# Kernel tuning notes

Hardware: AMD Instinct MI355X
Metric: run time of the kernel (lower is better)

## Reference

```python
import jax, jax.numpy as jnp
import numpy as np

N = 50000       # nodes
E = 600000      # directed edges (before self loops)
IN_CH = 128
HID = 64
HEADS = 2
H2_CH = HID // HEADS  # 32
OUT_CH = 96
NEG_SLOPE = 0.2


def _w(key, shape):
    fan_in = shape[-1]
    return jax.random.normal(key, shape, dtype=jnp.float32) / np.sqrt(fan_in).astype(np.float32)


def setup_inputs() -> dict:
    key = jax.random.key(0)
    ks = jax.random.split(key, 20)
    x = jax.random.normal(ks[0], (N, IN_CH), dtype=jnp.float32)
    edge_index = jax.random.randint(ks[1], (2, E), 0, N, dtype=jnp.int32)
    batch = jnp.zeros((N,), dtype=jnp.int32)
    return {
        "x": x, "edge_index": edge_index, "batch": batch,
        # lin_in 128->128
        "Win": _w(ks[2], (IN_CH, IN_CH)), "b_in": jnp.zeros((IN_CH,), jnp.float32),
        # conv1: GATv2Conv(128 -> 64, heads=2, concat=True)
        "Wl1": _w(ks[3], (HEADS * HID, IN_CH)), "bl1": jnp.zeros((HEADS * HID,), jnp.float32),
        "Wr1": _w(ks[4], (HEADS * HID, IN_CH)), "br1": jnp.zeros((HEADS * HID,), jnp.float32),
        "att1": _w(ks[5], (HEADS, HID)), "bias1": jnp.zeros((HEADS * HID,), jnp.float32),
        # conv2: GATv2Conv(128 -> 32, heads=1, concat=True)
        "Wl2": _w(ks[6], (H2_CH, HEADS * HID)), "bl2": jnp.zeros((H2_CH,), jnp.float32),
        "Wr2": _w(ks[7], (H2_CH, HEADS * HID)), "br2": jnp.zeros((H2_CH,), jnp.float32),
        "att2": _w(ks[8], (1, H2_CH)), "bias2": jnp.zeros((H2_CH,), jnp.float32),
        # final linear 32 -> 96
        "Wout": _w(ks[9], (OUT_CH, H2_CH)), "b_out": jnp.zeros((OUT_CH,), jnp.float32),
    }


def _segment_softmax(logits, seg, num):
    # logits: [E, H] grouped by seg (destination node); every node has a self loop.
    m = jax.ops.segment_max(logits, seg, num_segments=num)
    ex = jnp.exp(logits - m[seg])
    s = jax.ops.segment_sum(ex, seg, num_segments=num)
    return ex / s[seg]


def _gatv2_conv(h, Wl, bl, Wr, br, att, bias, src, dst, heads, ch):
    n = h.shape[0]
    xl = (h @ Wl.T + bl).reshape(n, heads, ch)  # source-side (x_j)
    xr = (h @ Wr.T + br).reshape(n, heads, ch)  # target-side (x_i)
    e = jax.nn.leaky_relu(xl[src] + xr[dst], NEG_SLOPE)       # [E, H, C]
    logits = jnp.einsum('ehc,hc->eh', e, att)                  # [E, H]
    alpha = _segment_softmax(logits, dst, n)                   # softmax over in-edges per dst
    out = jax.ops.segment_sum(alpha[:, :, None] * xl[src], dst, num_segments=n)
    return out.reshape(n, heads * ch) + bias


def reference(x, edge_index, batch, Win, b_in, Wl1, bl1, Wr1, br1, att1, bias1,
              Wl2, bl2, Wr2, br2, att2, bias2, Wout, b_out):
    n = x.shape[0]
    loops = jnp.arange(n, dtype=edge_index.dtype)
    src = jnp.concatenate([edge_index[0], loops])  # add_self_loops=True (PyG default)
    dst = jnp.concatenate([edge_index[1], loops])
    h = x @ Win.T + b_in
    h = jax.nn.relu(_gatv2_conv(h, Wl1, bl1, Wr1, br1, att1, bias1, src, dst, HEADS, HID))
    h = jax.nn.relu(_gatv2_conv(h, Wl2, bl2, Wr2, br2, att2, bias2, src, dst, 1, H2_CH))
    num_graphs = 1
    sums = jax.ops.segment_sum(h, batch, num_segments=num_graphs)          # [G, 32]
    cnt = jax.ops.segment_sum(jnp.ones((n,), h.dtype), batch, num_segments=num_graphs)
    pooled = sums / cnt[:, None]
    return pooled @ Wout.T + b_out  # [G, 96]
```

## Files before the change

kernel.cpp:

```cpp
#include <hip/hip_runtime.h>
#include <hip/hip_bf16.h>
#include <math.h>


#define NEG_SLOPE 0.2f
#define LOG2E 1.4426950408889634f
#define NREP 16
#define ELLW 64
#define CH 2048
#define CAPB 8192

typedef __attribute__((ext_vector_type(8))) short bf16x8;
typedef __attribute__((ext_vector_type(4))) float f32x4;

__device__ __forceinline__ float leaky(float t) { return fmaxf(t, NEG_SLOPE * t); }
__device__ __forceinline__ float bf2f(unsigned short u) {
    return __uint_as_float((unsigned)u << 16);
}
__device__ __forceinline__ short f2bf(float f) {
    __hip_bfloat16 h = __float2bfloat16(f);
    return *reinterpret_cast<short*>(&h);
}
__device__ __forceinline__ short f2bf_fast(float f) {
    return (short)((__float_as_uint(f) + 0x8000u) >> 16);
}

template <int CTRL>
__device__ __forceinline__ float dppadd(float v) {
    int t = __builtin_amdgcn_update_dpp(0, __float_as_int(v), CTRL, 0xF, 0xF, true);
    return v + __int_as_float(t);
}

__global__ __launch_bounds__(256) void prep_kernel(const float* __restrict__ Win,
                                                   const float* __restrict__ b_in,
                                                   const float* __restrict__ Wl1,
                                                   const float* __restrict__ bl1,
                                                   const float* __restrict__ Wr1,
                                                   const float* __restrict__ br1,
                                                   const float* __restrict__ Wl2,
                                                   const float* __restrict__ bl2,
                                                   const float* __restrict__ Wr2,
                                                   const float* __restrict__ br2,
                                                   unsigned short* __restrict__ Wcat1,
                                                   float* __restrict__ bcat1,
                                                   unsigned short* __restrict__ Wcat2,
                                                   float* __restrict__ bcat2,
                                                   int* __restrict__ bucketCnt,
                                                   float* __restrict__ pooledR, int N) {
    int b = blockIdx.x, t = threadIdx.x;
    if (b < 128) {
        int half = t >> 7;
        int k = t & 127;
        int o = b * 2 + half;
        const float* Wx = (o < 128) ? Wl1 : Wr1;
        const float* bx = (o < 128) ? bl1 : br1;
        int oo = o & 127;
        float acc = 0.f;
#pragma unroll 16
        for (int j = 0; j < 128; ++j)
            acc = fmaf(Wx[oo * 128 + j], Win[j * 128 + k], acc);
        Wcat1[o * 128 + k] = (unsigned short)f2bf(acc);

        __shared__ float red[256];
        red[t] = Wx[oo * 128 + k] * b_in[k];
        __syncthreads();
        for (int off = 64; off > 0; off >>= 1) {
            if (k < off) red[t] += red[t + off];
            __syncthreads();
        }
        if (k == 0) bcat1[o] = red[half * 128] + bx[oo];
    } else if (b < 160) {
        int i = (b - 128) * 256 + t;
        int m = i >> 7, kk = i & 127;
        float v = (m < 32) ? Wl2[m * 128 + kk] : Wr2[(m - 32) * 128 + kk];
        Wcat2[i] = (unsigned short)f2bf(v);
        if (b == 128 && t < 64) bcat2[t] = (t < 32) ? bl2[t] : br2[t - 32];
    } else if (b == 160) {
        if (t < 256) bucketCnt[t] = 0;
    } else {
        int i = (b - 161) * 256 + t;
        if (i < NREP * 32) pooledR[i] = 0.f;
    }
}

__device__ __forceinline__ void gemm1_body(const float* __restrict__ x,
                                           const unsigned short* __restrict__ W,
                                           const float* __restrict__ bias,
                                           unsigned short* __restrict__ XL,
                                           unsigned short* __restrict__ XR,
                                           int N, int nb) {
    const int w = threadIdx.x >> 6;
    const int lane = threadIdx.x & 63;
    const int ln = lane & 15;
    const int quad = lane >> 4;
    const int c0 = w * 64;

    int rows[2];
#pragma unroll
    for (int rt = 0; rt < 2; ++rt) {
        int n = nb + rt * 16 + ln;
        rows[rt] = n < N ? n : N - 1;
    }

    float4 araw[2][4][2];
#pragma unroll
    for (int rt = 0; rt < 2; ++rt)
#pragma unroll
        for (int kc = 0; kc < 4; ++kc) {
            const float* p = x + (size_t)rows[rt] * 128 + kc * 32 + quad * 8;
            araw[rt][kc][0] = *(const float4*)p;
            araw[rt][kc][1] = *(const float4*)(p + 4);
        }
    bf16x8 a[2][4];
#pragma unroll
    for (int rt = 0; rt < 2; ++rt)
#pragma unroll
        for (int kc = 0; kc < 4; ++kc) {
            float4 u = araw[rt][kc][0], v = araw[rt][kc][1];
            a[rt][kc][0] = f2bf_fast(u.x); a[rt][kc][1] = f2bf_fast(u.y);
            a[rt][kc][2] = f2bf_fast(u.z); a[rt][kc][3] = f2bf_fast(u.w);
            a[rt][kc][4] = f2bf_fast(v.x); a[rt][kc][5] = f2bf_fast(v.y);
            a[rt][kc][6] = f2bf_fast(v.z); a[rt][kc][7] = f2bf_fast(v.w);
        }

    f32x4 acc[2][4];
#pragma unroll
    for (int rt = 0; rt < 2; ++rt)
#pragma unroll
        for (int ct = 0; ct < 4; ++ct) acc[rt][ct] = (f32x4){0.f, 0.f, 0.f, 0.f};

#pragma unroll
    for (int kc = 0; kc < 4; ++kc) {
        const int k0 = kc * 32 + quad * 8;
        bf16x8 wv[4];
#pragma unroll
        for (int ct = 0; ct < 4; ++ct)
            wv[ct] = *(const bf16x8*)(W + (size_t)(c0 + ct * 16 + ln) * 128 + k0);
#pragma unroll
        for (int rt = 0; rt < 2; ++rt)
#pragma unroll
            for (int ct = 0; ct < 4; ++ct)
                acc[rt][ct] = __builtin_amdgcn_mfma_f32_16x16x32_bf16(wv[ct], a[rt][kc], acc[rt][ct], 0, 0, 0);
    }

#pragma unroll
    for (int rt = 0; rt < 2; ++rt) {
        int n = nb + rt * 16 + ln;
        if (n >= N) continue;
#pragma unroll
        for (int ct = 0; ct < 4; ++ct) {
            int cb = c0 + ct * 16 + quad * 4;
            float4 bv = *(const float4*)&bias[cb];
            ushort4 o;
            o.x = (unsigned short)f2bf(acc[rt][ct][0] + bv.x);
            o.y = (unsigned short)f2bf(acc[rt][ct][1] + bv.y);
            o.z = (unsigned short)f2bf(acc[rt][ct][2] + bv.z);
            o.w = (unsigned short)f2bf(acc[rt][ct][3] + bv.w);
            if (cb < 128) *(ushort4*)&XL[(size_t)n * 128 + cb] = o;
            else          *(ushort4*)&XR[(size_t)n * 128 + cb - 128] = o;
        }
    }
}

__global__ __launch_bounds__(256) void fuse1_kernel(const int* __restrict__ ei,
                                                    int* __restrict__ bucketCnt,
                                                    unsigned int* __restrict__ region,
                                                    int E,
                                                    const float* __restrict__ x,
                                                    const unsigned short* __restrict__ W,
                                                    const float* __restrict__ bias,
                                                    unsigned short* __restrict__ XL,
                                                    unsigned short* __restrict__ XR,
                                                    int N, int PB) {
    __shared__ int hist[256];
    __shared__ int base[256];
    __shared__ int off[256];
    if (blockIdx.x >= PB) {
        gemm1_body(x, W, bias, XL, XR, N, (blockIdx.x - PB) * 32);
        return;
    }
    int b = blockIdx.x, t = threadIdx.x;
    int e0 = b * CH;
    int e1 = e0 + CH; if (e1 > E) e1 = E;

    hist[t] = 0;
    __syncthreads();
    for (int e = e0 + t; e < e1; e += 256) {
        int d = ei[E + e];
        atomicAdd(&hist[d >> 8], 1);
    }
    __syncthreads();
    int h = hist[t];
    base[t] = (h > 0) ? atomicAdd(&bucketCnt[t], h) : 0;
    off[t] = 0;
    __syncthreads();
    for (int e = e0 + t; e < e1; e += 256) {
        int s = ei[e];
        int d = ei[E + e];
        int bk = d >> 8;
        int p = base[bk] + atomicAdd(&off[bk], 1);
        if (p < CAPB)
            region[(size_t)bk * CAPB + p] = (unsigned)s | ((unsigned)(d & 255) << 16);
    }
}

__global__ __launch_bounds__(256) void fuse2_kernel(const unsigned int* __restrict__ region,
                                                    const int* __restrict__ bucketCnt,
                                                    unsigned short* __restrict__ ell,
                                                    int* __restrict__ deg,
                                                    const float* __restrict__ x,
                                                    const unsigned short* __restrict__ W,
                                                    const float* __restrict__ bias,
                                                    unsigned short* __restrict__ XL,
                                                    unsigned short* __restrict__ XR,
                                                    int N, int NB, int nodeOff) {
    __shared__ unsigned short tile[256 * ELLW];
    __shared__ int cur[256];
    if (blockIdx.x >= NB) {
        gemm1_body(x, W, bias, XL, XR, N, nodeOff + (blockIdx.x - NB) * 32);
        return;
    }
    int nb = blockIdx.x, t = threadIdx.x;
    cur[t] = 0;
    __syncthreads();
    int cnt = bucketCnt[nb];
    if (cnt > CAPB) cnt = CAPB;
    for (int i = t; i < cnt; i += 256) {
        unsigned p = region[(size_t)nb * CAPB + i];
        int doff = p >> 16;
        int s = p & 0xFFFF;
        int r = atomicAdd(&cur[doff], 1);
        if (r < ELLW) tile[doff * ELLW + r] = (unsigned short)s;
    }
    __syncthreads();
    int node = nb * 256 + t;
    int dgl = cur[t];
    if (dgl > ELLW) dgl = ELLW;
    if (node < N) {
        deg[node] = dgl;
        int pe = dgl + 8; if (pe > ELLW) pe = ELLW;
        for (int r = dgl; r < pe; ++r) tile[t * ELLW + r] = (unsigned short)node;
    }
    __syncthreads();
    const uint4* tl = (const uint4*)tile;
    uint4* gl = (uint4*)(ell + (size_t)nb * 256 * ELLW);
#pragma unroll
    for (int k = 0; k < 8; ++k) {
        int idx = t + k * 256;
        int row = idx >> 3;
        if (nb * 256 + row < N) gl[idx] = tl[idx];
    }
}

__global__ __launch_bounds__(256) void node_conv1(const unsigned short* __restrict__ XL,
                                                  const unsigned short* __restrict__ XR,
                                                  const int* __restrict__ deg,
                                                  const unsigned short* __restrict__ ell,
                                                  const float* __restrict__ att,
                                                  const float* __restrict__ bias,
                                                  const unsigned short* __restrict__ Wcat2,
                                                  const float* __restrict__ bcat2,
                                                  unsigned short* __restrict__ XL2,
                                                  unsigned short* __restrict__ XR2, int N) {
    __shared__ unsigned short hsh[8 * 128];
    int g = threadIdx.x >> 5;
    int d = blockIdx.x * 8 + g;
    int l = threadIdx.x & 31;
    int c0 = 4 * l;

    if (d < N) {
        const unsigned short* row = ell + (size_t)d * ELLW;
        int re = deg[d];

        float4 attv = *(const float4*)&att[c0];
        attv.x *= LOG2E; attv.y *= LOG2E; attv.z *= LOG2E; attv.w *= LOG2E;
        ushort4 xru = *(const ushort4*)&XR[(size_t)d * 128 + c0];
        float xr0 = bf2f(xru.x), xr1 = bf2f(xru.y), xr2 = bf2f(xru.z), xr3 = bf2f(xru.w);

        float ssum, a0, a1, a2, a3;
        float w_self, xs0, xs1, xs2, xs3;

#define LOADX1(s) (*(const ushort4*)&XL[(size_t)(s) * 128 + c0])
#define PROC1(xu)                                                          \
    {                                                                      \
        float x0 = bf2f(xu.x), x1 = bf2f(xu.y), x2 = bf2f(xu.z), x3 = bf2f(xu.w); \
        float p = leaky(x0 + xr0) * attv.x;                                \
        p = fmaf(leaky(x1 + xr1), attv.y, p);                              \
        p = fmaf(leaky(x2 + xr2), attv.z, p);                              \
        p = fmaf(leaky(x3 + xr3), attv.w, p);                              \
        p = dppadd<0xB1>(p);                                               \
        p = dppadd<0x4E>(p);                                               \
        p = dppadd<0x124>(p);                                              \
        p = dppadd<0x128>(p);                                              \
        float wgt = exp2f(p);                                              \
        ssum += wgt;                                                       \
        a0 = fmaf(wgt, x0, a0); a1 = fmaf(wgt, x1, a1);                    \
        a2 = fmaf(wgt, x2, a2); a3 = fmaf(wgt, x3, a3);                    \
    }

        {
            ushort4 xu = *(const ushort4*)&XL[(size_t)d * 128 + c0];
            xs0 = bf2f(xu.x); xs1 = bf2f(xu.y); xs2 = bf2f(xu.z); xs3 = bf2f(xu.w);
            float p = leaky(xs0 + xr0) * attv.x;
            p = fmaf(leaky(xs1 + xr1), attv.y, p);
            p = fmaf(leaky(xs2 + xr2), attv.z, p);
            p = fmaf(leaky(xs3 + xr3), attv.w, p);
            p = dppadd<0xB1>(p);
            p = dppadd<0x4E>(p);
            p = dppadd<0x124>(p);
            p = dppadd<0x128>(p);
            w_self = exp2f(p);
            ssum = w_self;
            a0 = w_self * xs0; a1 = w_self * xs1;
            a2 = w_self * xs2; a3 = w_self * xs3;
        }
        if (re > 0) {
            int rp = (re + 3) & ~3;
            ushort4 i0 = *(const ushort4*)&row[0];
            ushort4 b0 = LOADX1(i0.x), b1 = LOADX1(i0.y), b2 = LOADX1(i0.z), b3 = LOADX1(i0.w);
            for (int j = 0; j < rp; j += 4) {
                int j4 = j + 4 < ELLW - 3 ? j + 4 : ELLW - 4;
                ushort4 i1 = *(const ushort4*)&row[j4];
                ushort4 n0 = LOADX1(i1.x), n1 = LOADX1(i1.y), n2 = LOADX1(i1.z), n3 = LOADX1(i1.w);
                PROC1(b0);
                PROC1(b1);
                PROC1(b2);
                PROC1(b3);
                b0 = n0; b1 = n1; b2 = n2; b3 = n3;
            }
            float kw = (float)(rp - re) * w_self;
            ssum -= kw;
            a0 = fmaf(-kw, xs0, a0); a1 = fmaf(-kw, xs1, a1);
            a2 = fmaf(-kw, xs2, a2); a3 = fmaf(-kw, xs3, a3);
        }
#undef PROC1
#undef LOADX1

        float inv = 1.0f / ssum;
        float4 bv = *(const float4*)&bias[c0];
        float r0 = fmaf(a0, inv, bv.x), r1 = fmaf(a1, inv, bv.y);
        float r2 = fmaf(a2, inv, bv.z), r3 = fmaf(a3, inv, bv.w);
        ushort4 o;
        o.x = (unsigned short)f2bf(r0 > 0.f ? r0 : 0.f);
        o.y = (unsigned short)f2bf(r1 > 0.f ? r1 : 0.f);
        o.z = (unsigned short)f2bf(r2 > 0.f ? r2 : 0.f);
        o.w = (unsigned short)f2bf(r3 > 0.f ? r3 : 0.f);
        *(ushort4*)&hsh[g * 128 + c0] = o;
    } else {
        *(ushort4*)&hsh[g * 128 + c0] = make_ushort4(0, 0, 0, 0);
    }
    __syncthreads();

    {
        int w = threadIdx.x >> 6;
        int lane = threadIdx.x & 63;
        int ln = lane & 15;
        int quad = lane >> 4;
        f32x4 acc = (f32x4){0.f, 0.f, 0.f, 0.f};
#pragma unroll
        for (int kc = 0; kc < 4; ++kc) {
            int k0 = kc * 32 + quad * 8;
            bf16x8 a;
            if (ln < 8) a = *(const bf16x8*)&hsh[ln * 128 + k0];
            else        a = (bf16x8){0, 0, 0, 0, 0, 0, 0, 0};
            bf16x8 wv = *(const bf16x8*)(Wcat2 + (size_t)(w * 16 + ln) * 128 + k0);
            acc = __builtin_amdgcn_mfma_f32_16x16x32_bf16(wv, a, acc, 0, 0, 0);
        }
        int n = blockIdx.x * 8 + ln;
        if (ln < 8 && n < N) {
            int cb = w * 16 + quad * 4;
            float4 bv = *(const float4*)&bcat2[cb];
            ushort4 o;
            o.x = (unsigned short)f2bf(acc[0] + bv.x);
            o.y = (unsigned short)f2bf(acc[1] + bv.y);
            o.z = (unsigned short)f2bf(acc[2] + bv.z);
            o.w = (unsigned short)f2bf(acc[3] + bv.w);
            if (cb < 32) *(ushort4*)&XL2[(size_t)n * 32 + cb] = o;
            else         *(ushort4*)&XR2[(size_t)n * 32 + cb - 32] = o;
        }
    }
}

__global__ __launch_bounds__(256) void node_conv2(const unsigned short* __restrict__ XL,
                                                  const unsigned short* __restrict__ XR,
                                                  const int* __restrict__ deg,
                                                  const unsigned short* __restrict__ ell,
                                                  const float* __restrict__ att,
                                                  const float* __restrict__ bias,
                                                  float* __restrict__ pooledR, int N) {
    __shared__ float psh[32];
    if (threadIdx.x < 32) psh[threadIdx.x] = 0.0f;
    __syncthreads();

    int slot = threadIdx.x >> 3;
    int l = threadIdx.x & 7;
    int c0 = 4 * l;
    float4 attv = *(const float4*)&att[c0];
    attv.x *= LOG2E; attv.y *= LOG2E; attv.z *= LOG2E; attv.w *= LOG2E;
    float4 bv = *(const float4*)&bias[c0];
    float p0 = 0.f, p1 = 0.f, p2 = 0.f, p3 = 0.f;

#define LOADX2(s) (*(const ushort4*)&XL[(size_t)(s) * 32 + c0])
#define PROC2(xu)                                                          \
    {                                                                      \
        float x0 = bf2f(xu.x), x1 = bf2f(xu.y), x2 = bf2f(xu.z), x3 = bf2f(xu.w); \
        float p = leaky(x0 + xr0) * attv.x;                                \
        p = fmaf(leaky(x1 + xr1), attv.y, p);                              \
        p = fmaf(leaky(x2 + xr2), attv.z, p);                              \
        p = fmaf(leaky(x3 + xr3), attv.w, p);                              \
        p = dppadd<0xB1>(p);                                               \
        p = dppadd<0x4E>(p);                                               \
        p = dppadd<0x141>(p);                                              \
        float wgt = exp2f(p);                                              \
        ssum += wgt;                                                       \
        a0 = fmaf(wgt, x0, a0); a1 = fmaf(wgt, x1, a1);                    \
        a2 = fmaf(wgt, x2, a2); a3 = fmaf(wgt, x3, a3);                    \
    }

    for (int d = blockIdx.x * 32 + slot; d < N; d += gridDim.x * 32) {
        const unsigned short* row = ell + (size_t)d * ELLW;
        int re = deg[d];
        ushort4 xru = *(const ushort4*)&XR[(size_t)d * 32 + c0];
        float xr0 = bf2f(xru.x), xr1 = bf2f(xru.y), xr2 = bf2f(xru.z), xr3 = bf2f(xru.w);
        float ssum, a0, a1, a2, a3;
        float w_self, xs0, xs1, xs2, xs3;

        {
            ushort4 xu = *(const ushort4*)&XL[(size_t)d * 32 + c0];
            xs0 = bf2f(xu.x); xs1 = bf2f(xu.y); xs2 = bf2f(xu.z); xs3 = bf2f(xu.w);
            float p = leaky(xs0 + xr0) * attv.x;
            p = fmaf(leaky(xs1 + xr1), attv.y, p);
            p = fmaf(leaky(xs2 + xr2), attv.z, p);
            p = fmaf(leaky(xs3 + xr3), attv.w, p);
            p = dppadd<0xB1>(p);
            p = dppadd<0x4E>(p);
            p = dppadd<0x141>(p);
            w_self = exp2f(p);
            ssum = w_self;
            a0 = w_self * xs0; a1 = w_self * xs1;
            a2 = w_self * xs2; a3 = w_self * xs3;
        }
        if (re > 0) {
            int rp = (re + 3) & ~3;
            ushort4 i0 = *(const ushort4*)&row[0];
            ushort4 b0 = LOADX2(i0.x), b1 = LOADX2(i0.y), b2 = LOADX2(i0.z), b3 = LOADX2(i0.w);
            for (int j = 0; j < rp; j += 4) {
                int j4 = j + 4 < ELLW - 3 ? j + 4 : ELLW - 4;
                ushort4 i1 = *(const ushort4*)&row[j4];
                ushort4 n0 = LOADX2(i1.x), n1 = LOADX2(i1.y), n2 = LOADX2(i1.z), n3 = LOADX2(i1.w);
                PROC2(b0);
                PROC2(b1);
                PROC2(b2);
                PROC2(b3);
                b0 = n0; b1 = n1; b2 = n2; b3 = n3;
            }
            float kw = (float)(rp - re) * w_self;
            ssum -= kw;
            a0 = fmaf(-kw, xs0, a0); a1 = fmaf(-kw, xs1, a1);
            a2 = fmaf(-kw, xs2, a2); a3 = fmaf(-kw, xs3, a3);
        }

        float inv = 1.0f / ssum;
        float r0 = fmaf(a0, inv, bv.x), r1 = fmaf(a1, inv, bv.y);
        float r2 = fmaf(a2, inv, bv.z), r3 = fmaf(a3, inv, bv.w);
        p0 += r0 > 0.f ? r0 : 0.f;
        p1 += r1 > 0.f ? r1 : 0.f;
        p2 += r2 > 0.f ? r2 : 0.f;
        p3 += r3 > 0.f ? r3 : 0.f;
    }
#undef PROC2
#undef LOADX2
    atomicAdd(&psh[c0 + 0], p0);
    atomicAdd(&psh[c0 + 1], p1);
    atomicAdd(&psh[c0 + 2], p2);
    atomicAdd(&psh[c0 + 3], p3);
    __syncthreads();
    float* rep = pooledR + (blockIdx.x & (NREP - 1)) * 32;
    if (threadIdx.x < 32) atomicAdd(&rep[threadIdx.x], psh[threadIdx.x]);
}

__global__ void out_kernel(const float* __restrict__ pooledR, const float* __restrict__ Wout,
                           const float* __restrict__ b_out, float* __restrict__ out, int N) {
    __shared__ float psum[32];
    if (threadIdx.x < 32) {
        float tot = 0.f;
#pragma unroll
        for (int r = 0; r < NREP; ++r) tot += pooledR[r * 32 + threadIdx.x];
        psum[threadIdx.x] = tot;
    }
    __syncthreads();
    int m = threadIdx.x;
    if (m < 96) {
        float invN = 1.0f / (float)N;
        float s = b_out[m];
#pragma unroll
        for (int c = 0; c < 32; ++c) s += (psum[c] * invN) * Wout[m * 32 + c];
        out[m] = s;
    }
}

extern "C" void kernel_launch(void* const* d_in, const int* in_sizes, int n_in,
                              void* d_out, int out_size, void* d_ws, size_t ws_size,
                              hipStream_t stream) {
    const float* x     = (const float*)d_in[0];
    const int*   ei    = (const int*)d_in[1];
    const float* Win   = (const float*)d_in[3];
    const float* b_in  = (const float*)d_in[4];
    const float* Wl1   = (const float*)d_in[5];
    const float* bl1   = (const float*)d_in[6];
    const float* Wr1   = (const float*)d_in[7];
    const float* br1   = (const float*)d_in[8];
    const float* att1  = (const float*)d_in[9];
    const float* bias1 = (const float*)d_in[10];
    const float* Wl2   = (const float*)d_in[11];
    const float* bl2   = (const float*)d_in[12];
    const float* Wr2   = (const float*)d_in[13];
    const float* br2   = (const float*)d_in[14];
    const float* att2  = (const float*)d_in[15];
    const float* bias2 = (const float*)d_in[16];
    const float* Wout  = (const float*)d_in[17];
    const float* b_out = (const float*)d_in[18];
    float* out = (float*)d_out;

    int N = in_sizes[0] / 128;
    int E = in_sizes[1] / 2;
    int NB = (N + 255) >> 8;

    char* wsb = (char*)d_ws;
    size_t off = 0;
    auto alloc = [&](size_t bytes) { void* p = wsb + off; off += (bytes + 255) & ~(size_t)255; return p; };

    unsigned short* XL1   = (unsigned short*)alloc((size_t)N * 128 * 2);
    unsigned short* XR1   = (unsigned short*)alloc((size_t)N * 128 * 2);
    unsigned short* XL2   = (unsigned short*)alloc((size_t)N * 32 * 2);
    unsigned short* XR2   = (unsigned short*)alloc((size_t)N * 32 * 2);
    unsigned short* Wcat1 = (unsigned short*)alloc(256 * 128 * 2);
    unsigned short* Wcat2 = (unsigned short*)alloc(64 * 128 * 2);
    float* bcat1   = (float*)alloc(256 * 4);
    float* bcat2   = (float*)alloc(64 * 4);
    float* pooledR = (float*)alloc(NREP * 32 * 4);
    int* bucketCnt = (int*)alloc(256 * 4);
    int* deg       = (int*)alloc((size_t)N * 4);
    unsigned int* region = (unsigned int*)alloc((size_t)NB * CAPB * 4);
    unsigned short* ell  = (unsigned short*)alloc((size_t)N * ELLW * 2);

    int PB  = (E + CH - 1) / CH;
    int GT  = (N + 31) / 32;
    int GB1 = GT / 2;
    int GB2 = GT - GB1;

    prep_kernel<<<163, 256, 0, stream>>>(Win, b_in, Wl1, bl1, Wr1, br1,
                                         Wl2, bl2, Wr2, br2,
                                         Wcat1, bcat1, Wcat2, bcat2, bucketCnt, pooledR, N);
    fuse1_kernel<<<PB + GB1, 256, 0, stream>>>(ei, bucketCnt, region, E,
                                               x, Wcat1, bcat1, XL1, XR1, N, PB);
    fuse2_kernel<<<NB + GB2, 256, 0, stream>>>(region, bucketCnt, ell, deg,
                                               x, Wcat1, bcat1, XL1, XR1, N, NB, GB1 * 32);
    node_conv1<<<(N + 7) / 8, 256, 0, stream>>>(XL1, XR1, deg, ell, att1, bias1,
                                                Wcat2, bcat2, XL2, XR2, N);
    node_conv2<<<GT, 256, 0, stream>>>(XL2, XR2, deg, ell, att2, bias2, pooledR, N);
    out_kernel<<<1, 128, 0, stream>>>(pooledR, Wout, b_out, out, N);
}
```

Measured before the change: 210.1 us.

## Sort destination nodes by in-degree to balance warps in attention kernels

Adds a counting sort of nodes by degree: fuse2 bins nodes by their ELL degree via shared and global atomics, and a new compact kernel concatenates the bins into an ordering array that packs node id and degree together. Both conv kernels now process nodes in this order, so warps and blocks handle nodes of similar degree and lose less time to divergence. It costs an extra kernel launch, extra global scatter traffic, and scattered writes of conv1 outputs. It also relies on node ids fitting in 16 bits, which holds for 50000 nodes.

```diff
diff --git a/kernel.cpp b/kernel.cpp
--- a/kernel.cpp
+++ b/kernel.cpp
@@ -9,6 +9,7 @@
 #define ELLW 64
 #define CH 2048
 #define CAPB 8192
+#define BINCAP 16384
 
 typedef __attribute__((ext_vector_type(8))) short bf16x8;
 typedef __attribute__((ext_vector_type(4))) float f32x4;
@@ -46,6 +47,7 @@
                                                    unsigned short* __restrict__ Wcat2,
                                                    float* __restrict__ bcat2,
                                                    int* __restrict__ bucketCnt,
+                                                   int* __restrict__ binCnt,
                                                    float* __restrict__ pooledR, int N) {
     int b = blockIdx.x, t = threadIdx.x;
     if (b < 128) {
@@ -76,7 +78,8 @@
         Wcat2[i] = (unsigned short)f2bf(v);
         if (b == 128 && t < 64) bcat2[t] = (t < 32) ? bl2[t] : br2[t - 32];
     } else if (b == 160) {
-        if (t < 256) bucketCnt[t] = 0;
+        bucketCnt[t] = 0;
+        binCnt[t] = 0;
     } else {
         int i = (b - 161) * 256 + t;
         if (i < NREP * 32) pooledR[i] = 0.f;
@@ -207,7 +210,8 @@
 __global__ __launch_bounds__(256) void fuse2_kernel(const unsigned int* __restrict__ region,
                                                     const int* __restrict__ bucketCnt,
                                                     unsigned short* __restrict__ ell,
-                                                    int* __restrict__ deg,
+                                                    int* __restrict__ binCnt,
+                                                    int* __restrict__ ordBins,
                                                     const float* __restrict__ x,
                                                     const unsigned short* __restrict__ W,
                                                     const float* __restrict__ bias,
@@ -216,12 +220,15 @@
                                                     int N, int NB, int nodeOff) {
     __shared__ unsigned short tile[256 * ELLW];
     __shared__ int cur[256];
+    __shared__ int bh[65];
+    __shared__ int bbase[65];
     if (blockIdx.x >= NB) {
         gemm1_body(x, W, bias, XL, XR, N, nodeOff + (blockIdx.x - NB) * 32);
         return;
     }
     int nb = blockIdx.x, t = threadIdx.x;
     cur[t] = 0;
+    if (t < 65) bh[t] = 0;
     __syncthreads();
     int cnt = bucketCnt[nb];
     if (cnt > CAPB) cnt = CAPB;
@@ -236,12 +243,14 @@
     int node = nb * 256 + t;
     int dgl = cur[t];
     if (dgl > ELLW) dgl = ELLW;
+    int lrank = -1;
     if (node < N) {
-        deg[node] = dgl;
         int pe = dgl + 8; if (pe > ELLW) pe = ELLW;
         for (int r = dgl; r < pe; ++r) tile[t * ELLW + r] = (unsigned short)node;
-    }
-    __syncthreads();
+        lrank = atomicAdd(&bh[dgl], 1);
+    }
+    __syncthreads();
+    if (t < 65 && bh[t] > 0) bbase[t] = atomicAdd(&binCnt[t], bh[t]);
     const uint4* tl = (const uint4*)tile;
     uint4* gl = (uint4*)(ell + (size_t)nb * 256 * ELLW);
 #pragma unroll
@@ -250,11 +259,34 @@
         int row = idx >> 3;
         if (nb * 256 + row < N) gl[idx] = tl[idx];
     }
+    __syncthreads();
+    if (lrank >= 0) {
+        int pos = bbase[dgl] + lrank;
+        if (pos < BINCAP) ordBins[(size_t)dgl * BINCAP + pos] = node;
+    }
+}
+
+__global__ __launch_bounds__(256) void compact_kernel(const int* __restrict__ binCnt,
+                                                      const int* __restrict__ ordBins,
+                                                      int* __restrict__ ord) {
+    __shared__ int cnts[65];
+    __shared__ int startS;
+    int b = blockIdx.x, t = threadIdx.x;
+    if (t < 65) cnts[t] = binCnt[t];
+    if (t == 0) startS = 0;
+    __syncthreads();
+    if (t < b) atomicAdd(&startS, cnts[t]);
+    __syncthreads();
+    int cnt = cnts[b]; if (cnt > BINCAP) cnt = BINCAP;
+    int start = startS;
+    int tag = b << 16;
+    for (int i = t; i < cnt; i += 256)
+        ord[start + i] = ordBins[(size_t)b * BINCAP + i] | tag;
 }
 
 __global__ __launch_bounds__(256) void node_conv1(const unsigned short* __restrict__ XL,
                                                   const unsigned short* __restrict__ XR,
-                                                  const int* __restrict__ deg,
+                                                  const int* __restrict__ ord,
                                                   const unsigned short* __restrict__ ell,
                                                   const float* __restrict__ att,
                                                   const float* __restrict__ bias,
@@ -263,14 +295,21 @@
                                                   unsigned short* __restrict__ XL2,
                                                   unsigned short* __restrict__ XR2, int N) {
     __shared__ unsigned short hsh[8 * 128];
+    __shared__ int dmap[8];
     int g = threadIdx.x >> 5;
-    int d = blockIdx.x * 8 + g;
     int l = threadIdx.x & 31;
     int c0 = 4 * l;
-
-    if (d < N) {
+    int i = blockIdx.x * 8 + g;
+    int d = -1, re = 0;
+    if (i < N) {
+        int u = ord[i];
+        d = u & 0xFFFF;
+        re = u >> 16;
+    }
+    if (l == 0) dmap[g] = d;
+
+    if (d >= 0) {
         const unsigned short* row = ell + (size_t)d * ELLW;
-        int re = deg[d];
 
         float4 attv = *(const float4*)&att[c0];
         attv.x *= LOG2E; attv.y *= LOG2E; attv.z *= LOG2E; attv.w *= LOG2E;
@@ -366,8 +405,8 @@
             bf16x8 wv = *(const bf16x8*)(Wcat2 + (size_t)(w * 16 + ln) * 128 + k0);
             acc = __builtin_amdgcn_mfma_f32_16x16x32_bf16(wv, a, acc, 0, 0, 0);
         }
-        int n = blockIdx.x * 8 + ln;
-        if (ln < 8 && n < N) {
+        int n = (ln < 8) ? dmap[ln] : -1;
+        if (n >= 0) {
             int cb = w * 16 + quad * 4;
             float4 bv = *(const float4*)&bcat2[cb];
             ushort4 o;
@@ -383,7 +422,7 @@
 
 __global__ __launch_bounds__(256) void node_conv2(const unsigned short* __restrict__ XL,
                                                   const unsigned short* __restrict__ XR,
-                                                  const int* __restrict__ deg,
+                                                  const int* __restrict__ ord,
                                                   const unsigned short* __restrict__ ell,
                                                   const float* __restrict__ att,
                                                   const float* __restrict__ bias,
@@ -395,9 +434,6 @@
     int slot = threadIdx.x >> 3;
     int l = threadIdx.x & 7;
     int c0 = 4 * l;
-    float4 attv = *(const float4*)&att[c0];
-    attv.x *= LOG2E; attv.y *= LOG2E; attv.z *= LOG2E; attv.w *= LOG2E;
-    float4 bv = *(const float4*)&bias[c0];
     float p0 = 0.f, p1 = 0.f, p2 = 0.f, p3 = 0.f;
 
 #define LOADX2(s) (*(const ushort4*)&XL[(size_t)(s) * 32 + c0])
@@ -417,9 +453,15 @@
         a2 = fmaf(wgt, x2, a2); a3 = fmaf(wgt, x3, a3);                    \
     }
 
-    for (int d = blockIdx.x * 32 + slot; d < N; d += gridDim.x * 32) {
+    int idx = blockIdx.x * 32 + slot;
+    if (idx < N) {
+        int u = ord[idx];
+        int d = u & 0xFFFF;
+        int re = u >> 16;
         const unsigned short* row = ell + (size_t)d * ELLW;
-        int re = deg[d];
+        float4 attv = *(const float4*)&att[c0];
+        attv.x *= LOG2E; attv.y *= LOG2E; attv.z *= LOG2E; attv.w *= LOG2E;
+        float4 bv = *(const float4*)&bias[c0];
         ushort4 xru = *(const ushort4*)&XR[(size_t)d * 32 + c0];
         float xr0 = bf2f(xru.x), xr1 = bf2f(xru.y), xr2 = bf2f(xru.z), xr3 = bf2f(xru.w);
         float ssum, a0, a1, a2, a3;
@@ -463,10 +505,10 @@
         float inv = 1.0f / ssum;
         float r0 = fmaf(a0, inv, bv.x), r1 = fmaf(a1, inv, bv.y);
         float r2 = fmaf(a2, inv, bv.z), r3 = fmaf(a3, inv, bv.w);
-        p0 += r0 > 0.f ? r0 : 0.f;
-        p1 += r1 > 0.f ? r1 : 0.f;
-        p2 += r2 > 0.f ? r2 : 0.f;
-        p3 += r3 > 0.f ? r3 : 0.f;
+        p0 = r0 > 0.f ? r0 : 0.f;
+        p1 = r1 > 0.f ? r1 : 0.f;
+        p2 = r2 > 0.f ? r2 : 0.f;
+        p3 = r3 > 0.f ? r3 : 0.f;
     }
 #undef PROC2
 #undef LOADX2
@@ -540,8 +582,10 @@
     float* bcat2   = (float*)alloc(64 * 4);
     float* pooledR = (float*)alloc(NREP * 32 * 4);
     int* bucketCnt = (int*)alloc(256 * 4);
-    int* deg       = (int*)alloc((size_t)N * 4);
+    int* binCnt    = (int*)alloc(256 * 4);
+    int* ord       = (int*)alloc((size_t)N * 4);
     unsigned int* region = (unsigned int*)alloc((size_t)NB * CAPB * 4);
+    int* ordBins   = (int*)alloc((size_t)65 * BINCAP * 4);
     unsigned short* ell  = (unsigned short*)alloc((size_t)N * ELLW * 2);
 
     int PB  = (E + CH - 1) / CH;
@@ -551,13 +595,14 @@
 
     prep_kernel<<<163, 256, 0, stream>>>(Win, b_in, Wl1, bl1, Wr1, br1,
                                          Wl2, bl2, Wr2, br2,
-                                         Wcat1, bcat1, Wcat2, bcat2, bucketCnt, pooledR, N);
+                                         Wcat1, bcat1, Wcat2, bcat2, bucketCnt, binCnt, pooledR, N);
     fuse1_kernel<<<PB + GB1, 256, 0, stream>>>(ei, bucketCnt, region, E,
                                                x, Wcat1, bcat1, XL1, XR1, N, PB);
-    fuse2_kernel<<<NB + GB2, 256, 0, stream>>>(region, bucketCnt, ell, deg,
+    fuse2_kernel<<<NB + GB2, 256, 0, stream>>>(region, bucketCnt, ell, binCnt, ordBins,
                                                x, Wcat1, bcat1, XL1, XR1, N, NB, GB1 * 32);
-    node_conv1<<<(N + 7) / 8, 256, 0, stream>>>(XL1, XR1, deg, ell, att1, bias1,
+    compact_kernel<<<65, 256, 0, stream>>>(binCnt, ordBins, ord);
+    node_conv1<<<(N + 7) / 8, 256, 0, stream>>>(XL1, XR1, ord, ell, att1, bias1,
                                                 Wcat2, bcat2, XL2, XR2, N);
-    node_conv2<<<GT, 256, 0, stream>>>(XL2, XR2, deg, ell, att2, bias2, pooledR, N);
+    node_conv2<<<GT, 256, 0, stream>>>(XL2, XR2, ord, ell, att2, bias2, pooledR, N);
     out_kernel<<<1, 128, 0, stream>>>(pooledR, Wout, b_out, out, N);
 }
```

Measured after the change: 218.2 us. +3.9%, slower.
